# Kernel optimization log

Hardware: AMD Instinct MI355X
Metric: run time of the kernel (lower is better)

Reference implementation:

```python
import math
import jax, jax.numpy as jnp
import numpy as np

N_FEATURES = 32
DEGREE = 3
BATCH = 8192
N_POLY = math.comb(N_FEATURES + DEGREE, DEGREE)  # 6545


def _build_monomial_indices(n_features, degree):
    """Static (numpy) indices replicating the Pascal-triangle recursion in TaylorMap._poly.

    For degree level i (i = 1..degree-1), the original code appends, for each feature f,
    x[:, f] * prev_block[:, :comb(i+f, i)].  We flatten that into gather index arrays so the
    whole block is one vectorized gather+multiply instead of a Python loop of slices/concats.
    """
    levels = []
    for i in range(1, degree):
        counts = np.array([math.comb(i + f, i) for f in range(n_features)], dtype=np.int64)
        f_idx = np.repeat(np.arange(n_features, dtype=np.int64), counts)
        m_idx = np.concatenate([np.arange(c, dtype=np.int64) for c in counts])
        levels.append((f_idx, m_idx))
    return levels

_LEVELS = _build_monomial_indices(N_FEATURES, DEGREE)


def _poly(x):
    # x: [B, n].  Returns [B, n_poly] monomial features in the exact order of TaylorMap._poly.
    b = x.shape[0]
    parts = [jnp.ones((b, 1), x.dtype), x]
    prev = x
    for f_idx, m_idx in _LEVELS:  # static loop over degree levels (degree-1 iterations)
        new = x[:, f_idx] * prev[:, m_idx]  # [B, comb(n+i, i+1)-ish block]
        parts.append(new)
        prev = new
    return jnp.concatenate(parts, axis=-1)


def setup_inputs() -> dict:
    key = jax.random.key(0)
    kx, kw = jax.random.split(key)
    x = jax.random.normal(kx, (BATCH, N_FEATURES), dtype=jnp.float32)
    # learned weight W: [n_poly, n_features] (default init is zeros; use small randn for a
    # non-degenerate numerical baseline)
    W = jax.random.normal(kw, (N_POLY, N_FEATURES), dtype=jnp.float32) * 0.02
    return {"x": x, "W": W}


def reference(x, W):
    # TaylorMap(x) = x * residual + poly(x) @ W   (residual=True)
    return x + _poly(x) @ W
```

## Files before the change

kernel.cpp:

```cpp
#include <hip/hip_runtime.h>
#include <cstdint>
#include <cstddef>
#include <utility>


#define NF 32
#define NPOLY 6545
#define KPAD 6656
#define CHUNK_K 416
#define STEPS 26

typedef _Float16 f16x8 __attribute__((ext_vector_type(8)));
typedef float f32x16 __attribute__((ext_vector_type(16)));

struct Tbl { uint32_t v[KPAD]; };

constexpr Tbl build_tbl() {
    Tbl t{};
    int k = 0;
    t.v[k++] = (0u << 18);
    for (int f = 0; f < NF; ++f)
        t.v[k++] = (1u << 18) | (uint32_t(f) << 12);
    for (int f = 0; f < NF; ++f)
        for (int m = 0; m <= f; ++m)
            t.v[k++] = (2u << 18) | (uint32_t(f) << 12) | (uint32_t(m) << 6);
    for (int f = 0; f < NF; ++f) {
        int cnt = (f + 1) * (f + 2) / 2;
        int g = 0, h = 0;
        for (int m = 0; m < cnt; ++m) {
            t.v[k++] = (3u << 18) | (uint32_t(f) << 12) | (uint32_t(g) << 6) | uint32_t(h);
            ++h;
            if (h > g) { ++g; h = 0; }
        }
    }
    while (k < KPAD) t.v[k++] = (7u << 18);
    return t;
}

constexpr Tbl TBL = build_tbl();

template<int K>
__device__ __forceinline__ float mono(const float (&xr)[NF]) {
    constexpr uint32_t e = TBL.v[K];
    constexpr int cnt = int(e >> 18);
    constexpr int a = int((e >> 12) & 63);
    constexpr int b = int((e >> 6) & 63);
    constexpr int c = int(e & 63);
    if constexpr (cnt == 0) return 1.0f;
    else if constexpr (cnt == 1) return xr[a];
    else if constexpr (cnt == 2) return xr[a] * xr[b];
    else if constexpr (cnt == 3) return (xr[a] * xr[b]) * xr[c];
    else return 0.0f;
}

template<int K0, int... Js>
__device__ __forceinline__ f16x8 gen_frag(const float (&xr)[NF], int hsel,
                                          std::integer_sequence<int, Js...>) {
    float lo[8] = { mono<K0 + Js>(xr)... };
    float hi[8] = { mono<K0 + 8 + Js>(xr)... };
    f16x8 r;
#pragma unroll
    for (int j = 0; j < 8; ++j)
        r[j] = (_Float16)(hsel ? hi[j] : lo[j]);
    return r;
}

template<int CB, int T>
__device__ __forceinline__ void step_one(const float (&xr)[NF], int hsel, int n,
                                         const _Float16* __restrict__ Wh,
                                         f32x16& acc) {
    constexpr int K0 = CB + T * 16;
    f16x8 a = gen_frag<K0>(xr, hsel, std::make_integer_sequence<int, 8>{});
    constexpr int TG = K0 >> 4;
    const f16x8* bp = (const f16x8*)(Wh + ((((TG * 2 + hsel) * 32) + n) << 3));
    f16x8 b = *bp;
    acc = __builtin_amdgcn_mfma_f32_32x32x16_f16(a, b, acc, 0, 0, 0);
}

template<int CB, int... Ts>
__device__ __forceinline__ void chunk_impl(std::integer_sequence<int, Ts...>,
                                           const float (&xr)[NF], int hsel, int n,
                                           const _Float16* __restrict__ Wh,
                                           f32x16& acc) {
    (step_one<CB, Ts>(xr, hsel, n, Wh, acc), ...);
}

template<int CB>
__device__ __forceinline__ void do_chunk(const float (&xr)[NF], int hsel, int n,
                                         const _Float16* __restrict__ Wh,
                                         f32x16& acc) {
    chunk_impl<CB>(std::make_integer_sequence<int, STEPS>{}, xr, hsel, n, Wh, acc);
}

__global__ void init_out(const float4* __restrict__ x, float4* __restrict__ out) {
    int id = blockIdx.x * 256 + threadIdx.x;
    out[id] = x[id];
}

__global__ void prep_w(const float* __restrict__ W, _Float16* __restrict__ Wh) {
    int id = blockIdx.x * 256 + threadIdx.x;
    int n = id & 31;
    int k = id >> 5;
    int t = k >> 4, kk = k & 15;
    int h = kk >> 3, j = kk & 7;
    float v = (k < NPOLY) ? W[k * 32 + n] : 0.0f;
    Wh[(((t * 2 + h) * 32 + n) << 3) + j] = (_Float16)v;
}

__global__ __launch_bounds__(256) void gemm(const float* __restrict__ x,
                                            const _Float16* __restrict__ Wh,
                                            float* __restrict__ out) {
    const int tid = threadIdx.x;
    const int wave = tid >> 6;
    const int lane = tid & 63;
    const int hsel = lane >> 5;
    const int m_local = lane & 31;
    const int mtile = blockIdx.x >> 2;
    const int cgroup = blockIdx.x & 3;
    const int chunk = cgroup * 4 + wave;

    const int row = mtile * 32 + m_local;
    float xr[NF];
    const float4* xp = (const float4*)(x + (size_t)row * NF);
#pragma unroll
    for (int i = 0; i < 8; ++i) {
        float4 v = xp[i];
        xr[4 * i + 0] = v.x; xr[4 * i + 1] = v.y;
        xr[4 * i + 2] = v.z; xr[4 * i + 3] = v.w;
    }

    f32x16 acc;
#pragma unroll
    for (int i = 0; i < 16; ++i) acc[i] = 0.0f;

    switch (chunk) {
        case  0: do_chunk< 0 * CHUNK_K>(xr, hsel, m_local, Wh, acc); break;
        case  1: do_chunk< 1 * CHUNK_K>(xr, hsel, m_local, Wh, acc); break;
        case  2: do_chunk< 2 * CHUNK_K>(xr, hsel, m_local, Wh, acc); break;
        case  3: do_chunk< 3 * CHUNK_K>(xr, hsel, m_local, Wh, acc); break;
        case  4: do_chunk< 4 * CHUNK_K>(xr, hsel, m_local, Wh, acc); break;
        case  5: do_chunk< 5 * CHUNK_K>(xr, hsel, m_local, Wh, acc); break;
        case  6: do_chunk< 6 * CHUNK_K>(xr, hsel, m_local, Wh, acc); break;
        case  7: do_chunk< 7 * CHUNK_K>(xr, hsel, m_local, Wh, acc); break;
        case  8: do_chunk< 8 * CHUNK_K>(xr, hsel, m_local, Wh, acc); break;
        case  9: do_chunk< 9 * CHUNK_K>(xr, hsel, m_local, Wh, acc); break;
        case 10: do_chunk<10 * CHUNK_K>(xr, hsel, m_local, Wh, acc); break;
        case 11: do_chunk<11 * CHUNK_K>(xr, hsel, m_local, Wh, acc); break;
        case 12: do_chunk<12 * CHUNK_K>(xr, hsel, m_local, Wh, acc); break;
        case 13: do_chunk<13 * CHUNK_K>(xr, hsel, m_local, Wh, acc); break;
        case 14: do_chunk<14 * CHUNK_K>(xr, hsel, m_local, Wh, acc); break;
        case 15: do_chunk<15 * CHUNK_K>(xr, hsel, m_local, Wh, acc); break;
        default: break;
    }

    __shared__ float red[4][32][32];
#pragma unroll
    for (int r = 0; r < 16; ++r) {
        int rr = (r & 3) + 8 * (r >> 2) + 4 * hsel;
        red[wave][rr][m_local] = acc[r];
    }
    __syncthreads();

#pragma unroll
    for (int i = 0; i < 4; ++i) {
        int e = tid + i * 256;
        int rr = e >> 5, cc = e & 31;
        float s = red[0][rr][cc] + red[1][rr][cc] + red[2][rr][cc] + red[3][rr][cc];
        atomicAdd(out + ((size_t)(mtile * 32 + rr) * 32 + cc), s);
    }
}

extern "C" void kernel_launch(void* const* d_in, const int* in_sizes, int n_in,
                              void* d_out, int out_size, void* d_ws, size_t ws_size,
                              hipStream_t stream) {
    (void)in_sizes; (void)n_in; (void)out_size; (void)ws_size;
    const float* x = (const float*)d_in[0];
    const float* W = (const float*)d_in[1];
    float* out = (float*)d_out;
    _Float16* Wh = (_Float16*)d_ws;

    init_out<<<256, 256, 0, stream>>>((const float4*)x, (float4*)out);
    prep_w<<<832, 256, 0, stream>>>(W, Wh);
    gemm<<<1024, 256, 0, stream>>>(x, Wh, out);
}
```

Measured before the change: 71.66 us.

## Precompute degree-2 monomials in shared memory and prefetch B fragments

Each block first computes the 528 degree-2 monomials per row once into LDS as fp16, so the GEMM waves read them and form degree-3 terms with one packed fp16 multiply instead of recomputing every product in fp32 registers. B fragments are double-buffered with prefetch two steps ahead, and sched barriers fix the ordering. prep_w is changed so each thread writes a vectorized 8-wide fp16 fragment. The cross-wave reduction now uses LDS atomics into one tile instead of four. This adds LDS traffic and bank-conflict risk, and computing degree-3 products in fp16 may cost accuracy.

```diff
diff --git a/kernel.cpp b/kernel.cpp
--- a/kernel.cpp
+++ b/kernel.cpp
@@ -9,8 +9,12 @@
 #define KPAD 6656
 #define CHUNK_K 416
 #define STEPS 26
+#define D2N 528
+#define D2STRIDE 530
+#define XSTRIDE 34
 
 typedef _Float16 f16x8 __attribute__((ext_vector_type(8)));
+typedef _Float16 f16x2 __attribute__((ext_vector_type(2)));
 typedef float f32x16 __attribute__((ext_vector_type(16)));
 
 struct Tbl { uint32_t v[KPAD]; };
@@ -36,60 +40,105 @@
     while (k < KPAD) t.v[k++] = (7u << 18);
     return t;
 }
-
 constexpr Tbl TBL = build_tbl();
 
+struct D2I { uint8_t a[D2N]; uint8_t b[D2N]; };
+constexpr D2I build_d2i() {
+    D2I t{};
+    int k = 0;
+    for (int f = 0; f < NF; ++f)
+        for (int m = 0; m <= f; ++m) { t.a[k] = (uint8_t)f; t.b[k] = (uint8_t)m; ++k; }
+    return t;
+}
+constexpr D2I D2T = build_d2i();
+
+template<int K> struct EK {
+    static constexpr uint32_t e = TBL.v[K];
+    static constexpr int cnt = int(e >> 18);
+    static constexpr int a = int((e >> 12) & 63);
+    static constexpr int b = int((e >> 6) & 63);
+    static constexpr int c = int(e & 63);
+    static constexpr int pm = (cnt == 3) ? (b * (b + 1) / 2 + c)
+                            : (cnt == 2) ? (a * (a + 1) / 2 + b) : 0;
+};
+
 template<int K>
-__device__ __forceinline__ float mono(const float (&xr)[NF]) {
-    constexpr uint32_t e = TBL.v[K];
-    constexpr int cnt = int(e >> 18);
-    constexpr int a = int((e >> 12) & 63);
-    constexpr int b = int((e >> 6) & 63);
-    constexpr int c = int(e & 63);
-    if constexpr (cnt == 0) return 1.0f;
-    else if constexpr (cnt == 1) return xr[a];
-    else if constexpr (cnt == 2) return xr[a] * xr[b];
-    else if constexpr (cnt == 3) return (xr[a] * xr[b]) * xr[c];
-    else return 0.0f;
-}
-
-template<int K0, int... Js>
-__device__ __forceinline__ f16x8 gen_frag(const float (&xr)[NF], int hsel,
-                                          std::integer_sequence<int, Js...>) {
-    float lo[8] = { mono<K0 + Js>(xr)... };
-    float hi[8] = { mono<K0 + 8 + Js>(xr)... };
+__device__ __forceinline__ _Float16 elem(const _Float16* xrow, const _Float16* d2row) {
+    using E = EK<K>;
+    if constexpr (E::cnt == 0) return (_Float16)1.0f;
+    else if constexpr (E::cnt == 1) return xrow[E::a];
+    else if constexpr (E::cnt == 2) return d2row[E::pm];
+    else if constexpr (E::cnt == 3) return xrow[E::a] * d2row[E::pm];
+    else return (_Float16)0.0f;
+}
+
+template<int K>
+__device__ __forceinline__ f16x2 pair2(const _Float16* xrow, const _Float16* d2row) {
+    using E1 = EK<K>; using E2 = EK<K + 1>;
+    if constexpr (E1::cnt == 3 && E2::cnt == 3 && E1::a == E2::a && E2::pm == E1::pm + 1) {
+        f16x2 dd = { d2row[E1::pm], d2row[E1::pm + 1] };
+        _Float16 xf = xrow[E1::a];
+        f16x2 xx = { xf, xf };
+        return dd * xx;
+    } else if constexpr (E1::cnt == 2 && E2::cnt == 2 && E2::pm == E1::pm + 1) {
+        f16x2 dd = { d2row[E1::pm], d2row[E1::pm + 1] };
+        return dd;
+    } else {
+        f16x2 r = { elem<K>(xrow, d2row), elem<K + 1>(xrow, d2row) };
+        return r;
+    }
+}
+
+template<int KB>
+__device__ __forceinline__ f16x8 gen8(const _Float16* xrow, const _Float16* d2row) {
+    f16x2 p0 = pair2<KB + 0>(xrow, d2row);
+    f16x2 p1 = pair2<KB + 2>(xrow, d2row);
+    f16x2 p2 = pair2<KB + 4>(xrow, d2row);
+    f16x2 p3 = pair2<KB + 6>(xrow, d2row);
     f16x8 r;
-#pragma unroll
-    for (int j = 0; j < 8; ++j)
-        r[j] = (_Float16)(hsel ? hi[j] : lo[j]);
+    r[0] = p0[0]; r[1] = p0[1]; r[2] = p1[0]; r[3] = p1[1];
+    r[4] = p2[0]; r[5] = p2[1]; r[6] = p3[0]; r[7] = p3[1];
     return r;
 }
 
 template<int CB, int T>
-__device__ __forceinline__ void step_one(const float (&xr)[NF], int hsel, int n,
-                                         const _Float16* __restrict__ Wh,
-                                         f32x16& acc) {
-    constexpr int K0 = CB + T * 16;
-    f16x8 a = gen_frag<K0>(xr, hsel, std::make_integer_sequence<int, 8>{});
-    constexpr int TG = K0 >> 4;
-    const f16x8* bp = (const f16x8*)(Wh + ((((TG * 2 + hsel) * 32) + n) << 3));
-    f16x8 b = *bp;
-    acc = __builtin_amdgcn_mfma_f32_32x32x16_f16(a, b, acc, 0, 0, 0);
+__device__ __forceinline__ f16x8 loadB(const _Float16* __restrict__ Wh, int hsel, int n) {
+    constexpr int TG = (CB + T * 16) >> 4;
+    return *(const f16x8*)(Wh + ((((TG * 2) + 0) * 32) * 8) + ((hsel * 32 + n) << 3));
 }
 
 template<int CB, int... Ts>
 __device__ __forceinline__ void chunk_impl(std::integer_sequence<int, Ts...>,
-                                           const float (&xr)[NF], int hsel, int n,
+                                           const _Float16* xrow, const _Float16* d2row,
                                            const _Float16* __restrict__ Wh,
-                                           f32x16& acc) {
-    (step_one<CB, Ts>(xr, hsel, n, Wh, acc), ...);
+                                           int hsel, int n, f32x16& acc) {
+    f16x8 bq[2];
+    bq[0] = loadB<CB, 0>(Wh, hsel, n);
+    bq[1] = loadB<CB, 1>(Wh, hsel, n);
+    ([&] {
+        constexpr int T = Ts;
+        f16x8 b = bq[T & 1];
+        if constexpr (T + 2 < STEPS) bq[T & 1] = loadB<CB, T + 2>(Wh, hsel, n);
+        constexpr int K0 = CB + T * 16;
+        f16x8 a;
+        if (hsel == 0) a = gen8<K0>(xrow, d2row);
+        else           a = gen8<K0 + 8>(xrow, d2row);
+        acc = __builtin_amdgcn_mfma_f32_32x32x16_f16(a, b, acc, 0, 0, 0);
+        __builtin_amdgcn_sched_barrier(0);
+    }(), ...);
 }
 
 template<int CB>
-__device__ __forceinline__ void do_chunk(const float (&xr)[NF], int hsel, int n,
+__device__ __forceinline__ void do_chunk(const _Float16* xrow, const _Float16* d2row,
                                          const _Float16* __restrict__ Wh,
-                                         f32x16& acc) {
-    chunk_impl<CB>(std::make_integer_sequence<int, STEPS>{}, xr, hsel, n, Wh, acc);
+                                         int hsel, int n, f32x16& acc) {
+    chunk_impl<CB>(std::make_integer_sequence<int, STEPS>{}, xrow, d2row, Wh, hsel, n, acc);
+}
+
+template<int M0, int... Ms>
+__device__ __forceinline__ void p1_impl(std::integer_sequence<int, Ms...>,
+                                        const float (&xr)[NF], _Float16* d2row) {
+    ((d2row[M0 + Ms] = (_Float16)(xr[D2T.a[M0 + Ms]] * xr[D2T.b[M0 + Ms]])), ...);
 }
 
 __global__ void init_out(const float4* __restrict__ x, float4* __restrict__ out) {
@@ -100,73 +149,104 @@
 __global__ void prep_w(const float* __restrict__ W, _Float16* __restrict__ Wh) {
     int id = blockIdx.x * 256 + threadIdx.x;
     int n = id & 31;
-    int k = id >> 5;
-    int t = k >> 4, kk = k & 15;
-    int h = kk >> 3, j = kk & 7;
-    float v = (k < NPOLY) ? W[k * 32 + n] : 0.0f;
-    Wh[(((t * 2 + h) * 32 + n) << 3) + j] = (_Float16)v;
+    int hh = (id >> 5) & 1;
+    int tg = id >> 6;
+    f16x8 v;
+#pragma unroll
+    for (int j = 0; j < 8; ++j) {
+        int k = tg * 16 + hh * 8 + j;
+        float w = (k < NPOLY) ? W[k * 32 + n] : 0.0f;
+        v[j] = (_Float16)w;
+    }
+    *(f16x8*)(Wh + (size_t)id * 8) = v;
 }
 
 __global__ __launch_bounds__(256) void gemm(const float* __restrict__ x,
                                             const _Float16* __restrict__ Wh,
                                             float* __restrict__ out) {
+    __shared__ __align__(16) _Float16 xh[32 * XSTRIDE];
+    __shared__ __align__(16) _Float16 d2h[32 * D2STRIDE];
+    __shared__ __align__(16) float red[32 * 32];
+
     const int tid = threadIdx.x;
     const int wave = tid >> 6;
     const int lane = tid & 63;
     const int hsel = lane >> 5;
-    const int m_local = lane & 31;
+    const int n = lane & 31;
     const int mtile = blockIdx.x >> 2;
     const int cgroup = blockIdx.x & 3;
     const int chunk = cgroup * 4 + wave;
 
-    const int row = mtile * 32 + m_local;
-    float xr[NF];
-    const float4* xp = (const float4*)(x + (size_t)row * NF);
-#pragma unroll
-    for (int i = 0; i < 8; ++i) {
-        float4 v = xp[i];
-        xr[4 * i + 0] = v.x; xr[4 * i + 1] = v.y;
-        xr[4 * i + 2] = v.z; xr[4 * i + 3] = v.w;
-    }
+#pragma unroll
+    for (int i = 0; i < 4; ++i) red[tid + i * 256] = 0.0f;
+
+    {
+        const int prow = tid & 31;
+        const int G = tid >> 5;
+        float xr[NF];
+        const float4* xp = (const float4*)(x + (size_t)(mtile * 32 + prow) * NF);
+#pragma unroll
+        for (int i = 0; i < 8; ++i) {
+            float4 v = xp[i];
+            xr[4 * i + 0] = v.x; xr[4 * i + 1] = v.y;
+            xr[4 * i + 2] = v.z; xr[4 * i + 3] = v.w;
+        }
+        _Float16* xrow_w = xh + prow * XSTRIDE;
+#pragma unroll
+        for (int i = 0; i < 4; ++i) xrow_w[G * 4 + i] = (_Float16)xr[G * 4 + i];
+        _Float16* d2row_w = d2h + prow * D2STRIDE;
+        switch (G) {
+            case 0: p1_impl<0 * 66>(std::make_integer_sequence<int, 66>{}, xr, d2row_w); break;
+            case 1: p1_impl<1 * 66>(std::make_integer_sequence<int, 66>{}, xr, d2row_w); break;
+            case 2: p1_impl<2 * 66>(std::make_integer_sequence<int, 66>{}, xr, d2row_w); break;
+            case 3: p1_impl<3 * 66>(std::make_integer_sequence<int, 66>{}, xr, d2row_w); break;
+            case 4: p1_impl<4 * 66>(std::make_integer_sequence<int, 66>{}, xr, d2row_w); break;
+            case 5: p1_impl<5 * 66>(std::make_integer_sequence<int, 66>{}, xr, d2row_w); break;
+            case 6: p1_impl<6 * 66>(std::make_integer_sequence<int, 66>{}, xr, d2row_w); break;
+            case 7: p1_impl<7 * 66>(std::make_integer_sequence<int, 66>{}, xr, d2row_w); break;
+            default: break;
+        }
+    }
+    __syncthreads();
+
+    const _Float16* xrow = xh + n * XSTRIDE;
+    const _Float16* d2row = d2h + n * D2STRIDE;
 
     f32x16 acc;
 #pragma unroll
     for (int i = 0; i < 16; ++i) acc[i] = 0.0f;
 
     switch (chunk) {
-        case  0: do_chunk< 0 * CHUNK_K>(xr, hsel, m_local, Wh, acc); break;
-        case  1: do_chunk< 1 * CHUNK_K>(xr, hsel, m_local, Wh, acc); break;
-        case  2: do_chunk< 2 * CHUNK_K>(xr, hsel, m_local, Wh, acc); break;
-        case  3: do_chunk< 3 * CHUNK_K>(xr, hsel, m_local, Wh, acc); break;
-        case  4: do_chunk< 4 * CHUNK_K>(xr, hsel, m_local, Wh, acc); break;
-        case  5: do_chunk< 5 * CHUNK_K>(xr, hsel, m_local, Wh, acc); break;
-        case  6: do_chunk< 6 * CHUNK_K>(xr, hsel, m_local, Wh, acc); break;
-        case  7: do_chunk< 7 * CHUNK_K>(xr, hsel, m_local, Wh, acc); break;
-        case  8: do_chunk< 8 * CHUNK_K>(xr, hsel, m_local, Wh, acc); break;
-        case  9: do_chunk< 9 * CHUNK_K>(xr, hsel, m_local, Wh, acc); break;
-        case 10: do_chunk<10 * CHUNK_K>(xr, hsel, m_local, Wh, acc); break;
-        case 11: do_chunk<11 * CHUNK_K>(xr, hsel, m_local, Wh, acc); break;
-        case 12: do_chunk<12 * CHUNK_K>(xr, hsel, m_local, Wh, acc); break;
-        case 13: do_chunk<13 * CHUNK_K>(xr, hsel, m_local, Wh, acc); break;
-        case 14: do_chunk<14 * CHUNK_K>(xr, hsel, m_local, Wh, acc); break;
-        case 15: do_chunk<15 * CHUNK_K>(xr, hsel, m_local, Wh, acc); break;
+        case  0: do_chunk< 0 * CHUNK_K>(xrow, d2row, Wh, hsel, n, acc); break;
+        case  1: do_chunk< 1 * CHUNK_K>(xrow, d2row, Wh, hsel, n, acc); break;
+        case  2: do_chunk< 2 * CHUNK_K>(xrow, d2row, Wh, hsel, n, acc); break;
+        case  3: do_chunk< 3 * CHUNK_K>(xrow, d2row, Wh, hsel, n, acc); break;
+        case  4: do_chunk< 4 * CHUNK_K>(xrow, d2row, Wh, hsel, n, acc); break;
+        case  5: do_chunk< 5 * CHUNK_K>(xrow, d2row, Wh, hsel, n, acc); break;
+        case  6: do_chunk< 6 * CHUNK_K>(xrow, d2row, Wh, hsel, n, acc); break;
+        case  7: do_chunk< 7 * CHUNK_K>(xrow, d2row, Wh, hsel, n, acc); break;
+        case  8: do_chunk< 8 * CHUNK_K>(xrow, d2row, Wh, hsel, n, acc); break;
+        case  9: do_chunk< 9 * CHUNK_K>(xrow, d2row, Wh, hsel, n, acc); break;
+        case 10: do_chunk<10 * CHUNK_K>(xrow, d2row, Wh, hsel, n, acc); break;
+        case 11: do_chunk<11 * CHUNK_K>(xrow, d2row, Wh, hsel, n, acc); break;
+        case 12: do_chunk<12 * CHUNK_K>(xrow, d2row, Wh, hsel, n, acc); break;
+        case 13: do_chunk<13 * CHUNK_K>(xrow, d2row, Wh, hsel, n, acc); break;
+        case 14: do_chunk<14 * CHUNK_K>(xrow, d2row, Wh, hsel, n, acc); break;
+        case 15: do_chunk<15 * CHUNK_K>(xrow, d2row, Wh, hsel, n, acc); break;
         default: break;
     }
 
-    __shared__ float red[4][32][32];
 #pragma unroll
     for (int r = 0; r < 16; ++r) {
         int rr = (r & 3) + 8 * (r >> 2) + 4 * hsel;
-        red[wave][rr][m_local] = acc[r];
+        atomicAdd(&red[rr * 32 + n], acc[r]);
     }
     __syncthreads();
 
 #pragma unroll
     for (int i = 0; i < 4; ++i) {
         int e = tid + i * 256;
-        int rr = e >> 5, cc = e & 31;
-        float s = red[0][rr][cc] + red[1][rr][cc] + red[2][rr][cc] + red[3][rr][cc];
-        atomicAdd(out + ((size_t)(mtile * 32 + rr) * 32 + cc), s);
+        atomicAdd(out + ((size_t)(mtile * 32 + (e >> 5)) * 32 + (e & 31)), red[e]);
     }
 }
 
@@ -180,6 +260,6 @@
     _Float16* Wh = (_Float16*)d_ws;
 
     init_out<<<256, 256, 0, stream>>>((const float4*)x, (float4*)out);
-    prep_w<<<832, 256, 0, stream>>>(W, Wh);
+    prep_w<<<104, 256, 0, stream>>>(W, Wh);
     gemm<<<1024, 256, 0, stream>>>(x, Wh, out);
 }
```

Result: slower. 98.52 us (+37.5%).

## Factor cubic monomials as x_f times shared quadratic table in LDS

Applied to the files above, without the earlier changes.

Instead of recomputing every degree-1..3 monomial in registers per MFMA step, each block builds a per-row table of degree-0..2 terms in fp16 in swizzled LDS once. Cubic fragments are formed as one LDS vector read times a broadcast feature value, driven by a step descriptor table. The weight layout is reordered to match, with padding per feature group. The two prep kernels are merged into one launch, and the weight loads are double-buffered in the main loop. This trades heavy per-step VALU monomial generation for LDS traffic and a rebalanced step split. It adds an fp16 rounding of the quadratic terms before the multiply by x_f.

```diff
diff --git a/kernel.cpp b/kernel.cpp
--- a/kernel.cpp
+++ b/kernel.cpp
@@ -6,167 +6,206 @@
 
 #define NF 32
 #define NPOLY 6545
-#define KPAD 6656
-#define CHUNK_K 416
-#define STEPS 26
+#define NSTEPS 417
+#define NOCT 834
+#define TSTRIDE 576
+#define D2OFF 40
+#define XDSTRIDE 34
 
 typedef _Float16 f16x8 __attribute__((ext_vector_type(8)));
 typedef float f32x16 __attribute__((ext_vector_type(16)));
 
-struct Tbl { uint32_t v[KPAD]; };
-
-constexpr Tbl build_tbl() {
-    Tbl t{};
+#define D2N 528
+struct D2I { uint8_t a[D2N]; uint8_t b[D2N]; };
+constexpr D2I build_d2i() {
+    D2I t{};
     int k = 0;
-    t.v[k++] = (0u << 18);
     for (int f = 0; f < NF; ++f)
-        t.v[k++] = (1u << 18) | (uint32_t(f) << 12);
-    for (int f = 0; f < NF; ++f)
-        for (int m = 0; m <= f; ++m)
-            t.v[k++] = (2u << 18) | (uint32_t(f) << 12) | (uint32_t(m) << 6);
+        for (int m = 0; m <= f; ++m) { t.a[k] = (uint8_t)f; t.b[k] = (uint8_t)m; ++k; }
+    return t;
+}
+constexpr D2I D2T = build_d2i();
+
+struct Desc { uint32_t d[NOCT]; };
+constexpr Desc build_desc() {
+    Desc D{};
+    int u = 0;
+    for (int o = 0; o < 72; ++o)
+        D.d[u++] = (uint32_t)(o * 8);
     for (int f = 0; f < NF; ++f) {
         int cnt = (f + 1) * (f + 2) / 2;
-        int g = 0, h = 0;
-        for (int m = 0; m < cnt; ++m) {
-            t.v[k++] = (3u << 18) | (uint32_t(f) << 12) | (uint32_t(g) << 6) | uint32_t(h);
-            ++h;
-            if (h > g) { ++g; h = 0; }
+        for (int j8 = 0; j8 < (cnt + 7) / 8; ++j8)
+            D.d[u++] = (uint32_t)(D2OFF + 8 * j8) | ((uint32_t)(1 + f) << 16);
+    }
+    return D;
+}
+__device__ const Desc DESC_G = build_desc();
+
+struct Oldk { int16_t v[NSTEPS * 16]; };
+constexpr Oldk build_oldk() {
+    Oldk K{};
+    int k = 0;
+    for (int ti = 0; ti < 576; ++ti) {
+        int old;
+        if (ti == 0) old = 0;
+        else if (ti <= 32) old = ti;
+        else if (ti >= D2OFF && ti < D2OFF + D2N) old = 33 + (ti - D2OFF);
+        else old = -1;
+        K.v[k++] = (int16_t)old;
+    }
+    for (int f = 0; f < NF; ++f) {
+        int cnt = (f + 1) * (f + 2) / 2;
+        int off3 = 0;
+        for (int g = 0; g < f; ++g) off3 += (g + 1) * (g + 2) / 2;
+        int oc = (cnt + 7) / 8;
+        for (int m = 0; m < oc * 8; ++m)
+            K.v[k++] = (int16_t)(m < cnt ? 561 + off3 + m : -1);
+    }
+    return K;
+}
+__device__ const Oldk OLDK_G = build_oldk();
+
+template<int TI>
+__device__ __forceinline__ _Float16 tval(const float (&xr)[NF]) {
+    if constexpr (TI == 0) return (_Float16)1.0f;
+    else if constexpr (TI >= 1 && TI <= 32) return (_Float16)xr[TI - 1];
+    else if constexpr (TI >= D2OFF && TI < D2OFF + D2N) {
+        constexpr int m = TI - D2OFF;
+        return (_Float16)(xr[D2T.a[m]] * xr[D2T.b[m]]);
+    } else return (_Float16)0.0f;
+}
+
+template<int O, int... Js>
+__device__ __forceinline__ void put_oct(std::integer_sequence<int, Js...>,
+                                        const float (&xr)[NF], _Float16* trow, int r) {
+    f16x8 v = { tval<O * 8 + Js>(xr)... };
+    int slot = (O & ~7) | ((O ^ r) & 7);
+    *(f16x8*)(trow + slot * 8) = v;
+}
+
+template<int V>
+__device__ __forceinline__ void xdw(const float (&xr)[NF], _Float16* xdrow) {
+    if constexpr (V == 0) xdrow[0] = (_Float16)1.0f;
+    else xdrow[V] = (_Float16)xr[V - 1];
+}
+
+template<int G, int... Os>
+__device__ __forceinline__ void p1_group(std::integer_sequence<int, Os...>,
+                                         const float (&xr)[NF], _Float16* trow,
+                                         _Float16* xdrow, int r) {
+    (put_oct<9 * G + Os>(std::make_integer_sequence<int, 8>{}, xr, trow, r), ...);
+    xdw<4 * G + 0>(xr, xdrow); xdw<4 * G + 1>(xr, xdrow);
+    xdw<4 * G + 2>(xr, xdrow); xdw<4 * G + 3>(xr, xdrow);
+    if constexpr (G == 7) xdw<32>(xr, xdrow);
+}
+
+__global__ void prep(const float* __restrict__ x, const float* __restrict__ W,
+                     float* __restrict__ out, _Float16* __restrict__ Wh) {
+    int b = blockIdx.x;
+    if (b < 256) {
+        int id = b * 256 + threadIdx.x;
+        ((float4*)out)[id] = ((const float4*)x)[id];
+    } else {
+        int id = (b - 256) * 256 + threadIdx.x;
+        if (id < NSTEPS * 2 * 32) {
+            int step = id >> 6, rem = id & 63, hs = rem >> 5, n = rem & 31;
+            int k0 = step * 16 + hs * 8;
+            f16x8 v;
+#pragma unroll
+            for (int j = 0; j < 8; ++j) {
+                int old = OLDK_G.v[k0 + j];
+                v[j] = (_Float16)(old >= 0 ? W[old * 32 + n] : 0.0f);
+            }
+            *(f16x8*)(Wh + (size_t)id * 8) = v;
         }
     }
-    while (k < KPAD) t.v[k++] = (7u << 18);
-    return t;
-}
-
-constexpr Tbl TBL = build_tbl();
-
-template<int K>
-__device__ __forceinline__ float mono(const float (&xr)[NF]) {
-    constexpr uint32_t e = TBL.v[K];
-    constexpr int cnt = int(e >> 18);
-    constexpr int a = int((e >> 12) & 63);
-    constexpr int b = int((e >> 6) & 63);
-    constexpr int c = int(e & 63);
-    if constexpr (cnt == 0) return 1.0f;
-    else if constexpr (cnt == 1) return xr[a];
-    else if constexpr (cnt == 2) return xr[a] * xr[b];
-    else if constexpr (cnt == 3) return (xr[a] * xr[b]) * xr[c];
-    else return 0.0f;
-}
-
-template<int K0, int... Js>
-__device__ __forceinline__ f16x8 gen_frag(const float (&xr)[NF], int hsel,
-                                          std::integer_sequence<int, Js...>) {
-    float lo[8] = { mono<K0 + Js>(xr)... };
-    float hi[8] = { mono<K0 + 8 + Js>(xr)... };
-    f16x8 r;
-#pragma unroll
-    for (int j = 0; j < 8; ++j)
-        r[j] = (_Float16)(hsel ? hi[j] : lo[j]);
-    return r;
-}
-
-template<int CB, int T>
-__device__ __forceinline__ void step_one(const float (&xr)[NF], int hsel, int n,
-                                         const _Float16* __restrict__ Wh,
-                                         f32x16& acc) {
-    constexpr int K0 = CB + T * 16;
-    f16x8 a = gen_frag<K0>(xr, hsel, std::make_integer_sequence<int, 8>{});
-    constexpr int TG = K0 >> 4;
-    const f16x8* bp = (const f16x8*)(Wh + ((((TG * 2 + hsel) * 32) + n) << 3));
-    f16x8 b = *bp;
-    acc = __builtin_amdgcn_mfma_f32_32x32x16_f16(a, b, acc, 0, 0, 0);
-}
-
-template<int CB, int... Ts>
-__device__ __forceinline__ void chunk_impl(std::integer_sequence<int, Ts...>,
-                                           const float (&xr)[NF], int hsel, int n,
-                                           const _Float16* __restrict__ Wh,
-                                           f32x16& acc) {
-    (step_one<CB, Ts>(xr, hsel, n, Wh, acc), ...);
-}
-
-template<int CB>
-__device__ __forceinline__ void do_chunk(const float (&xr)[NF], int hsel, int n,
-                                         const _Float16* __restrict__ Wh,
-                                         f32x16& acc) {
-    chunk_impl<CB>(std::make_integer_sequence<int, STEPS>{}, xr, hsel, n, Wh, acc);
-}
-
-__global__ void init_out(const float4* __restrict__ x, float4* __restrict__ out) {
-    int id = blockIdx.x * 256 + threadIdx.x;
-    out[id] = x[id];
-}
-
-__global__ void prep_w(const float* __restrict__ W, _Float16* __restrict__ Wh) {
-    int id = blockIdx.x * 256 + threadIdx.x;
-    int n = id & 31;
-    int k = id >> 5;
-    int t = k >> 4, kk = k & 15;
-    int h = kk >> 3, j = kk & 7;
-    float v = (k < NPOLY) ? W[k * 32 + n] : 0.0f;
-    Wh[(((t * 2 + h) * 32 + n) << 3) + j] = (_Float16)v;
 }
 
 __global__ __launch_bounds__(256) void gemm(const float* __restrict__ x,
                                             const _Float16* __restrict__ Wh,
                                             float* __restrict__ out) {
+    __shared__ __align__(16) unsigned char smem[39040];
+    _Float16* t  = (_Float16*)smem;
+    _Float16* xd = (_Float16*)(smem + 36864);
+    float* red   = (float*)smem;
+
     const int tid = threadIdx.x;
-    const int wave = tid >> 6;
-    const int lane = tid & 63;
-    const int hsel = lane >> 5;
-    const int m_local = lane & 31;
-    const int mtile = blockIdx.x >> 2;
-    const int cgroup = blockIdx.x & 3;
-    const int chunk = cgroup * 4 + wave;
-
-    const int row = mtile * 32 + m_local;
-    float xr[NF];
-    const float4* xp = (const float4*)(x + (size_t)row * NF);
-#pragma unroll
-    for (int i = 0; i < 8; ++i) {
-        float4 v = xp[i];
-        xr[4 * i + 0] = v.x; xr[4 * i + 1] = v.y;
-        xr[4 * i + 2] = v.z; xr[4 * i + 3] = v.w;
-    }
+    const int wave = tid >> 6, lane = tid & 63;
+    const int hsel = lane >> 5, r = lane & 31;
+    const int mtile = blockIdx.x >> 2, cg = blockIdx.x & 3;
+
+    {
+        const int pr = tid & 31, g = tid >> 5;
+        float xr[NF];
+        const float4* xp = (const float4*)(x + (size_t)(mtile * 32 + pr) * NF);
+#pragma unroll
+        for (int i = 0; i < 8; ++i) {
+            float4 v = xp[i];
+            xr[4 * i + 0] = v.x; xr[4 * i + 1] = v.y;
+            xr[4 * i + 2] = v.z; xr[4 * i + 3] = v.w;
+        }
+        _Float16* trow = t + pr * TSTRIDE;
+        _Float16* xdrow = xd + pr * XDSTRIDE;
+        switch (g) {
+            case 0: p1_group<0>(std::make_integer_sequence<int, 9>{}, xr, trow, xdrow, pr); break;
+            case 1: p1_group<1>(std::make_integer_sequence<int, 9>{}, xr, trow, xdrow, pr); break;
+            case 2: p1_group<2>(std::make_integer_sequence<int, 9>{}, xr, trow, xdrow, pr); break;
+            case 3: p1_group<3>(std::make_integer_sequence<int, 9>{}, xr, trow, xdrow, pr); break;
+            case 4: p1_group<4>(std::make_integer_sequence<int, 9>{}, xr, trow, xdrow, pr); break;
+            case 5: p1_group<5>(std::make_integer_sequence<int, 9>{}, xr, trow, xdrow, pr); break;
+            case 6: p1_group<6>(std::make_integer_sequence<int, 9>{}, xr, trow, xdrow, pr); break;
+            default: p1_group<7>(std::make_integer_sequence<int, 9>{}, xr, trow, xdrow, pr); break;
+        }
+    }
+    __syncthreads();
+
+    const int c = cg * 4 + wave;
+    const int s0 = __builtin_amdgcn_readfirstlane((c * NSTEPS) >> 4);
+    const int s1 = __builtin_amdgcn_readfirstlane(((c + 1) * NSTEPS) >> 4);
+    const _Float16* trow = t + r * TSTRIDE;
+    const _Float16* xdrow = xd + r * XDSTRIDE;
+    const _Float16* wp = Wh + (size_t)lane * 8;
 
     f32x16 acc;
 #pragma unroll
     for (int i = 0; i < 16; ++i) acc[i] = 0.0f;
 
-    switch (chunk) {
-        case  0: do_chunk< 0 * CHUNK_K>(xr, hsel, m_local, Wh, acc); break;
-        case  1: do_chunk< 1 * CHUNK_K>(xr, hsel, m_local, Wh, acc); break;
-        case  2: do_chunk< 2 * CHUNK_K>(xr, hsel, m_local, Wh, acc); break;
-        case  3: do_chunk< 3 * CHUNK_K>(xr, hsel, m_local, Wh, acc); break;
-        case  4: do_chunk< 4 * CHUNK_K>(xr, hsel, m_local, Wh, acc); break;
-        case  5: do_chunk< 5 * CHUNK_K>(xr, hsel, m_local, Wh, acc); break;
-        case  6: do_chunk< 6 * CHUNK_K>(xr, hsel, m_local, Wh, acc); break;
-        case  7: do_chunk< 7 * CHUNK_K>(xr, hsel, m_local, Wh, acc); break;
-        case  8: do_chunk< 8 * CHUNK_K>(xr, hsel, m_local, Wh, acc); break;
-        case  9: do_chunk< 9 * CHUNK_K>(xr, hsel, m_local, Wh, acc); break;
-        case 10: do_chunk<10 * CHUNK_K>(xr, hsel, m_local, Wh, acc); break;
-        case 11: do_chunk<11 * CHUNK_K>(xr, hsel, m_local, Wh, acc); break;
-        case 12: do_chunk<12 * CHUNK_K>(xr, hsel, m_local, Wh, acc); break;
-        case 13: do_chunk<13 * CHUNK_K>(xr, hsel, m_local, Wh, acc); break;
-        case 14: do_chunk<14 * CHUNK_K>(xr, hsel, m_local, Wh, acc); break;
-        case 15: do_chunk<15 * CHUNK_K>(xr, hsel, m_local, Wh, acc); break;
-        default: break;
-    }
-
-    __shared__ float red[4][32][32];
-#pragma unroll
-    for (int r = 0; r < 16; ++r) {
-        int rr = (r & 3) + 8 * (r >> 2) + 4 * hsel;
-        red[wave][rr][m_local] = acc[r];
-    }
+    uint32_t dlo = DESC_G.d[2 * s0];
+    uint32_t dhi = DESC_G.d[2 * s0 + 1];
+    f16x8 b0 = *(const f16x8*)(wp + (size_t)s0 * 512);
+    f16x8 b1 = *(const f16x8*)(wp + (size_t)(s0 + 1) * 512);
+
+    for (int s = s0; s < s1; ++s) {
+        uint32_t d = hsel ? dhi : dlo;
+        dlo = DESC_G.d[2 * (s + 1)];
+        dhi = DESC_G.d[2 * (s + 1) + 1];
+        int toff = (int)(d & 0xffffu);
+        int xv = (int)(d >> 16);
+        int o = toff >> 3;
+        int slot = (o & ~7) | ((o ^ r) & 7);
+        f16x8 araw = *(const f16x8*)(trow + slot * 8);
+        _Float16 xs = xdrow[xv];
+        f16x8 xsv = { xs, xs, xs, xs, xs, xs, xs, xs };
+        f16x8 a = araw * xsv;
+        f16x8 bu = b0; b0 = b1;
+        b1 = *(const f16x8*)(wp + (size_t)(s + 2) * 512);
+        acc = __builtin_amdgcn_mfma_f32_32x32x16_f16(a, bu, acc, 0, 0, 0);
+    }
+
     __syncthreads();
-
+    float* bank = red + wave * 1024;
+#pragma unroll
+    for (int reg = 0; reg < 16; ++reg) {
+        int rr = (reg & 3) + 8 * (reg >> 2) + 4 * hsel;
+        bank[rr * 32 + r] = acc[reg];
+    }
+    __syncthreads();
+    float* op = out + (size_t)mtile * 1024;
 #pragma unroll
     for (int i = 0; i < 4; ++i) {
         int e = tid + i * 256;
-        int rr = e >> 5, cc = e & 31;
-        float s = red[0][rr][cc] + red[1][rr][cc] + red[2][rr][cc] + red[3][rr][cc];
-        atomicAdd(out + ((size_t)(mtile * 32 + rr) * 32 + cc), s);
+        float v = red[e] + red[1024 + e] + red[2048 + e] + red[3072 + e];
+        atomicAdd(op + e, v);
     }
 }
 
@@ -179,7 +218,6 @@
     float* out = (float*)d_out;
     _Float16* Wh = (_Float16*)d_ws;
 
-    init_out<<<256, 256, 0, stream>>>((const float4*)x, (float4*)out);
-    prep_w<<<832, 256, 0, stream>>>(W, Wh);
+    prep<<<361, 256, 0, stream>>>(x, W, out, Wh);
     gemm<<<1024, 256, 0, stream>>>(x, Wh, out);
 }
```

After: 74.23 us. +3.6%, slower.
